# Kernel optimization log

Measured on AMD Instinct MI355X. Metric: run time of the kernel, lower is better.

## Reference

```python
import jax, jax.numpy as jnp
import numpy as np

EMBED = 1024
HEADS = 16
HEAD_DIM = EMBED // HEADS
B, S = 2, 2048


def setup_inputs() -> dict:
    key = jax.random.key(0)
    ks = jax.random.split(key, 9)
    std = 1.0 / np.sqrt(EMBED)
    def lin(k):
        kw, kb = jax.random.split(k)
        W = jax.random.uniform(kw, (EMBED, EMBED), jnp.float32, -std, std)
        b = jax.random.uniform(kb, (EMBED,), jnp.float32, -std, std)
        return W, b
    Wq, bq = lin(ks[0])
    Wk, bk = lin(ks[1])
    Wv, bv = lin(ks[2])
    Wo, bo = lin(ks[3])
    x = jax.random.normal(ks[4], (B, S, EMBED), jnp.float32)
    return {"x": x, "Wq": Wq, "bq": bq, "Wk": Wk, "bk": bk,
            "Wv": Wv, "bv": bv, "Wo": Wo, "bo": bo}


def reference(x, Wq, bq, Wk, bk, Wv, bv, Wo, bo):
    b, s, e = x.shape
    # projections (torch Linear: x @ W^T + b; here W stored as [in,out])
    Q = x @ Wq + bq
    K = x @ Wk + bk
    V = x @ Wv + bv
    # [b, h, s, d]
    Q = Q.reshape(b, s, HEADS, HEAD_DIM).transpose(0, 2, 1, 3)
    K = K.reshape(b, s, HEADS, HEAD_DIM).transpose(0, 2, 1, 3)
    V = V.reshape(b, s, HEADS, HEAD_DIM).transpose(0, 2, 1, 3)
    scores = jnp.einsum('bhqd,bhkd->bhqk', Q, K) / np.sqrt(HEAD_DIM)
    # causal mask: positions k > q masked to -inf
    causal = jnp.tril(jnp.ones((s, s), dtype=bool))
    scores = jnp.where(causal[None, None], scores, -jnp.inf)
    weights = jax.nn.softmax(scores, axis=-1)
    out = jnp.einsum('bhqk,bhkd->bhqd', weights, V)
    out = out.transpose(0, 2, 1, 3).reshape(b, s, e)
    return out @ Wo + bo
```

## Files before the change

### kernel.cpp

```cpp
#include <hip/hip_runtime.h>
#include <hip/hip_bf16.h>
#include <stdint.h>

#define EMBED 1024
#define HEADS 16
#define HDIM 64
#define BATCH 2
#define SEQ 2048
#define NROWS (BATCH*SEQ)

typedef __attribute__((ext_vector_type(8))) short short8;
typedef __attribute__((ext_vector_type(4))) float f32x4;

#define LOG2E 1.44269504088896f

__device__ __forceinline__ unsigned short f2bf(float f) {
    __hip_bfloat16 b = __float2bfloat16(f);
    return *reinterpret_cast<unsigned short*>(&b);
}

__device__ __forceinline__ unsigned cvt_pk_bf16(float lo, float hi) {
    unsigned r;
    asm("v_cvt_pk_bf16_f32 %0, %1, %2" : "=v"(r) : "v"(lo), "v"(hi));
    return r;
}

__device__ __forceinline__ short8 mk8(unsigned a, unsigned b, unsigned c, unsigned d) {
    union { unsigned u[4]; short8 s; } x;
    x.u[0] = a; x.u[1] = b; x.u[2] = c; x.u[3] = d;
    return x.s;
}

__device__ __forceinline__ void g2l16(const void* g, void* l) {
    __builtin_amdgcn_global_load_lds(
        (const __attribute__((address_space(1))) unsigned int*)g,
        (__attribute__((address_space(3))) unsigned int*)l, 16, 0, 0);
}

__global__ void cast_x_kernel(const float* __restrict__ x,
                              unsigned short* __restrict__ xb, int n4) {
    int i = blockIdx.x * blockDim.x + threadIdx.x;
    if (i < n4) {
        float4 v = reinterpret_cast<const float4*>(x)[i];
        ushort4 o;
        o.x = f2bf(v.x); o.y = f2bf(v.y); o.z = f2bf(v.z); o.w = f2bf(v.w);
        reinterpret_cast<ushort4*>(xb)[i] = o;
    }
}

__global__ void transW4_kernel(const float* __restrict__ W0,
                               const float* __restrict__ W1,
                               const float* __restrict__ W2,
                               const float* __restrict__ W3,
                               unsigned short* __restrict__ dst) {
    __shared__ float tile[32][33];
    const int z = blockIdx.z;
    const float* W = (z == 0) ? W0 : (z == 1) ? W1 : (z == 2) ? W2 : W3;
    unsigned short* Wt = dst + (size_t)z * EMBED * EMBED;
    int tx = threadIdx.x, ty = threadIdx.y;
#pragma unroll
    for (int r = 0; r < 4; r++) {
        int i = blockIdx.y * 32 + ty + r * 8;
        int o = blockIdx.x * 32 + tx;
        tile[ty + r * 8][tx] = W[(size_t)i * EMBED + o];
    }
    __syncthreads();
    int i2 = blockIdx.y * 32 + tx;
#pragma unroll
    for (int r = 0; r < 4; r++) {
        int o2 = blockIdx.x * 32 + ty + r * 8;
        Wt[(size_t)o2 * EMBED + i2] = f2bf(tile[tx][ty + r * 8]);
    }
}

template<int MODE, int BM>
__global__ __launch_bounds__(256)
void gemm_kernel(const unsigned short* __restrict__ A,
                 const unsigned short* __restrict__ B,
                 int K,
                 unsigned short* __restrict__ Qo,
                 unsigned short* __restrict__ Ko,
                 unsigned short* __restrict__ Vto,
                 const float* __restrict__ bq,
                 const float* __restrict__ bk,
                 const float* __restrict__ bvv,
                 float* __restrict__ Co,
                 const float* __restrict__ bo) {
    constexpr int AI = BM / 32;
    __shared__ __attribute__((aligned(16))) unsigned short As[BM * 64];
    __shared__ __attribute__((aligned(16))) unsigned short Bs[128 * 64];
    const int t = threadIdx.x;
    const int lane = t & 63;
    const int w = t >> 6;
    const int wr = w >> 1, wc = w & 1;
    const int l15 = lane & 15, l16 = lane >> 4;
    const int m0 = blockIdx.y * BM;
    const int n0 = blockIdx.x * 128;

    f32x4 acc[AI][4];
#pragma unroll
    for (int i = 0; i < AI; i++)
#pragma unroll
        for (int j = 0; j < 4; j++) acc[i][j] = (f32x4){0.f, 0.f, 0.f, 0.f};

    for (int k0 = 0; k0 < K; k0 += 64) {
        __syncthreads();
#pragma unroll
        for (int i = 0; i < BM / 32; i++) {
            int c = i * 256 + t;
            int row = c >> 3;
            int lc = (c & 7) ^ (row & 7);
            g2l16(A + (size_t)(m0 + row) * K + k0 + lc * 8,
                  As + (size_t)(i * 256 + (t & ~63)) * 8);
        }
#pragma unroll
        for (int i = 0; i < 4; i++) {
            int c = i * 256 + t;
            int row = c >> 3;
            int lc = (c & 7) ^ (row & 7);
            g2l16(B + (size_t)(n0 + row) * K + k0 + lc * 8,
                  Bs + (size_t)(i * 256 + (t & ~63)) * 8);
        }
        __syncthreads();
#pragma unroll
        for (int kk = 0; kk < 2; kk++) {
            short8 a[AI], b[4];
#pragma unroll
            for (int ai = 0; ai < AI; ai++) {
                int row = wr * (BM / 2) + ai * 16 + l15;
                int ch = kk * 4 + l16;
                a[ai] = *reinterpret_cast<const short8*>(
                    As + row * 64 + ((ch ^ (row & 7)) << 3));
            }
#pragma unroll
            for (int bj = 0; bj < 4; bj++) {
                int row = wc * 64 + bj * 16 + l15;
                int ch = kk * 4 + l16;
                b[bj] = *reinterpret_cast<const short8*>(
                    Bs + row * 64 + ((ch ^ (row & 7)) << 3));
            }
            __builtin_amdgcn_s_setprio(1);
#pragma unroll
            for (int ai = 0; ai < AI; ai++)
#pragma unroll
                for (int bj = 0; bj < 4; bj++)
                    acc[ai][bj] = __builtin_amdgcn_mfma_f32_16x16x32_bf16(
                        a[ai], b[bj], acc[ai][bj], 0, 0, 0);
            __builtin_amdgcn_s_setprio(0);
        }
    }

    if (MODE == 0) {
        const int which = n0 >> 10;
        const int coln = n0 & 1023;
        const float* bias = which == 0 ? bq : (which == 1 ? bk : bvv);
        const float scale = which == 0 ? 0.125f * LOG2E : 1.0f;
#pragma unroll
        for (int ai = 0; ai < AI; ai++) {
            int rowb = m0 + wr * (BM / 2) + ai * 16 + l16 * 4;
            int b_ = rowb >> 11;
            int s = rowb & 2047;
#pragma unroll
            for (int bj = 0; bj < 4; bj++) {
                int col = coln + wc * 64 + bj * 16 + l15;
                float bsv = bias[col];
                int h = col >> 6, d = col & 63;
                if (which < 2) {
                    unsigned short* dst = (which == 0) ? Qo : Ko;
                    size_t base = ((size_t)(b_ * HEADS + h)) * SEQ * HDIM;
#pragma unroll
                    for (int r = 0; r < 4; r++) {
                        float v = (acc[ai][bj][r] + bsv) * scale;
                        dst[base + (size_t)(s + r) * HDIM + d] = f2bf(v);
                    }
                } else {
                    ushort4 pk;
                    pk.x = f2bf(acc[ai][bj][0] + bsv);
                    pk.y = f2bf(acc[ai][bj][1] + bsv);
                    pk.z = f2bf(acc[ai][bj][2] + bsv);
                    pk.w = f2bf(acc[ai][bj][3] + bsv);
                    int cs = (s >> 2) & 15;
                    int ps = (cs & 8) | ((cs & 3) << 1) | ((cs >> 2) & 1);
                    size_t off = ((size_t)(b_ * HEADS + h) * HDIM + d) * SEQ +
                                 (size_t)((s & ~63) | (ps << 2));
                    *reinterpret_cast<ushort4*>(Vto + off) = pk;
                }
            }
        }
    } else {
#pragma unroll
        for (int ai = 0; ai < AI; ai++) {
            int rowb = m0 + wr * (BM / 2) + ai * 16 + l16 * 4;
#pragma unroll
            for (int bj = 0; bj < 4; bj++) {
                int col = n0 + wc * 64 + bj * 16 + l15;
                float bsv = bo[col];
#pragma unroll
                for (int r = 0; r < 4; r++)
                    Co[(size_t)(rowb + r) * EMBED + col] = acc[ai][bj][r] + bsv;
            }
        }
    }
}

__device__ __forceinline__ void stage_kv(const unsigned short* __restrict__ Kg,
                                         const unsigned short* __restrict__ Vg,
                                         int kv0, unsigned short* Ksb,
                                         unsigned short* Vsb, int tl) {
#pragma unroll
    for (int i = 0; i < 4; i++) {
        int c = i * 128 + tl;
        int row = c >> 3;
        int lc = (c & 7) ^ (row & 7);
        g2l16(Kg + (size_t)(kv0 + row) * HDIM + lc * 8,
              Ksb + (i * 128 + (tl & ~63)) * 8);
    }
#pragma unroll
    for (int i = 0; i < 4; i++) {
        int c = i * 128 + tl;
        int d = c >> 3;
        int lc = (c & 7) ^ (d & 7);
        g2l16(Vg + (size_t)d * SEQ + kv0 + lc * 8,
              Vsb + (i * 128 + (tl & ~63)) * 8);
    }
}

__global__ __launch_bounds__(256, 2)
void attn_kernel(const unsigned short* __restrict__ Q,
                 const unsigned short* __restrict__ Kk,
                 const unsigned short* __restrict__ Vt,
                 unsigned short* __restrict__ O) {
    __shared__ __attribute__((aligned(16))) unsigned short Ks[4][64 * 64];
    __shared__ __attribute__((aligned(16))) unsigned short Vs[4][64 * 64];

    const int t = threadIdx.x;
    const int lane = t & 63;
    const int w = t >> 6;
    const int wq = w >> 1;
    const int wk = w & 1;
    const int l15 = lane & 15, l16 = lane >> 4;

    const int id = blockIdx.x;
    const int xcd = id & 7;
    const int u = id >> 3;
    const int bh = xcd * 4 + (u & 3);
    const int su = u >> 2;
    const int qi = (su < 16) ? su : 47 - su;
    const int q0 = qi * 64;
    const size_t base = (size_t)bh * SEQ * HDIM;
    const unsigned short* Kg = Kk + base;
    const unsigned short* Vg = Vt + base;
    const int qrow0 = q0 + wq * 32;

    short8 qf[2][2];
    {
        const unsigned short* Qg = Q + base + (size_t)qrow0 * HDIM;
#pragma unroll
        for (int qb = 0; qb < 2; qb++)
#pragma unroll
            for (int kc = 0; kc < 2; kc++)
                qf[qb][kc] = *reinterpret_cast<const short8*>(
                    Qg + (qb * 16 + l15) * HDIM + (kc * 4 + l16) * 8);
    }

    f32x4 oacc[2][4];
#pragma unroll
    for (int qb = 0; qb < 2; qb++)
#pragma unroll
        for (int nd = 0; nd < 4; nd++) oacc[qb][nd] = (f32x4){0.f, 0.f, 0.f, 0.f};
    float m_run[2] = {-1e30f, -1e30f};
    float l_run[2] = {0.f, 0.f};

    const int nt = qi + 1;
    const int nsuper = (nt + 1) >> 1;

    auto stagepair = [&](int ta, int tb) {
        if (t < 128) {
            if (ta < nt) stage_kv(Kg, Vg, ta * 64, Ks[ta & 3], Vs[ta & 3], t);
        } else {
            if (tb < nt) stage_kv(Kg, Vg, tb * 64, Ks[tb & 3], Vs[tb & 3], t - 128);
        }
    };

    auto qkt = [&](f32x4 (&sc)[2][4], const unsigned short* Kb) {
#pragma unroll
        for (int qb = 0; qb < 2; qb++)
#pragma unroll
            for (int kb = 0; kb < 4; kb++) sc[qb][kb] = (f32x4){0.f, 0.f, 0.f, 0.f};
#pragma unroll
        for (int kc = 0; kc < 2; kc++) {
            short8 ka[4];
#pragma unroll
            for (int kb = 0; kb < 4; kb++) {
                int row = kb * 16 + l15;
                ka[kb] = *reinterpret_cast<const short8*>(
                    Kb + row * 64 + (((kc * 4 + l16) ^ (row & 7)) << 3));
            }
            __builtin_amdgcn_s_setprio(1);
#pragma unroll
            for (int qb = 0; qb < 2; qb++)
#pragma unroll
                for (int kb = 0; kb < 4; kb++)
                    sc[qb][kb] = __builtin_amdgcn_mfma_f32_16x16x32_bf16(
                        ka[kb], qf[qb][kc], sc[qb][kb], 0, 0, 0);
            __builtin_amdgcn_s_setprio(0);
        }
    };

    auto softmax_pv = [&](f32x4 (&sc)[2][4], const unsigned short* Vb, bool diag) {
        if (diag) {
#pragma unroll
            for (int qb = 0; qb < 2; qb++) {
                const int qloc = wq * 32 + qb * 16 + l15;
#pragma unroll
                for (int kb = 0; kb < 4; kb++)
#pragma unroll
                    for (int r = 0; r < 4; r++) {
                        int kloc = kb * 16 + l16 * 4 + r;
                        sc[qb][kb][r] = (kloc > qloc) ? -1e30f : sc[qb][kb][r];
                    }
            }
        }
        float vmax[2];
        bool need = false;
#pragma unroll
        for (int qb = 0; qb < 2; qb++) {
            float mx = -1e30f;
#pragma unroll
            for (int kb = 0; kb < 4; kb++)
                mx = fmaxf(mx, fmaxf(fmaxf(sc[qb][kb][0], sc[qb][kb][1]),
                                     fmaxf(sc[qb][kb][2], sc[qb][kb][3])));
            mx = fmaxf(mx, __shfl_xor(mx, 16));
            mx = fmaxf(mx, __shfl_xor(mx, 32));
            vmax[qb] = mx;
            need = need || (mx > m_run[qb] + 8.0f);
        }
        if (__any(need)) {
#pragma unroll
            for (int qb = 0; qb < 2; qb++) {
                float mn = fmaxf(m_run[qb], vmax[qb]);
                float sf = __builtin_amdgcn_exp2f(m_run[qb] - mn);
                m_run[qb] = mn;
                l_run[qb] *= sf;
#pragma unroll
                for (int r = 0; r < 4; r++) {
                    float sfr = __shfl(sf, l16 * 4 + r);
#pragma unroll
                    for (int nd = 0; nd < 4; nd++) oacc[qb][nd][r] *= sfr;
                }
            }
        }
        short8 pa[2][2];
#pragma unroll
        for (int qb = 0; qb < 2; qb++) {
            float p[4][4];
            float ps = 0.f;
#pragma unroll
            for (int kb = 0; kb < 4; kb++)
#pragma unroll
                for (int r = 0; r < 4; r++) {
                    p[kb][r] = __builtin_amdgcn_exp2f(sc[qb][kb][r] - m_run[qb]);
                    ps += p[kb][r];
                }
            pa[qb][0] = mk8(cvt_pk_bf16(p[0][0], p[0][1]),
                            cvt_pk_bf16(p[0][2], p[0][3]),
                            cvt_pk_bf16(p[1][0], p[1][1]),
                            cvt_pk_bf16(p[1][2], p[1][3]));
            pa[qb][1] = mk8(cvt_pk_bf16(p[2][0], p[2][1]),
                            cvt_pk_bf16(p[2][2], p[2][3]),
                            cvt_pk_bf16(p[3][0], p[3][1]),
                            cvt_pk_bf16(p[3][2], p[3][3]));
            ps += __shfl_xor(ps, 16);
            ps += __shfl_xor(ps, 32);
            l_run[qb] += ps;
        }
#pragma unroll
        for (int m = 0; m < 2; m++) {
            short8 vb[4];
#pragma unroll
            for (int nd = 0; nd < 4; nd++) {
                int row = nd * 16 + l15;
                vb[nd] = *reinterpret_cast<const short8*>(
                    Vb + row * 64 + (((m * 4 + l16) ^ (row & 7)) << 3));
            }
            __builtin_amdgcn_s_setprio(1);
#pragma unroll
            for (int qb = 0; qb < 2; qb++)
#pragma unroll
                for (int nd = 0; nd < 4; nd++)
                    oacc[qb][nd] = __builtin_amdgcn_mfma_f32_16x16x32_bf16(
                        pa[qb][m], vb[nd], oacc[qb][nd], 0, 0, 0);
            __builtin_amdgcn_s_setprio(0);
        }
    };

    f32x4 sc[2][4];

    stagepair(0, 1);
    asm volatile("s_waitcnt vmcnt(0)" ::: "memory");
    __builtin_amdgcn_s_barrier();
    asm volatile("" ::: "memory");
    stagepair(2, 3);
    int myt = wk;
    if (myt < nt) qkt(sc, Ks[myt & 3]);

    for (int j = 1; j < nsuper; j++) {
        if (myt < nt) softmax_pv(sc, Vs[myt & 3], false);
        asm volatile("s_waitcnt vmcnt(0)" ::: "memory");
        __builtin_amdgcn_s_barrier();
        asm volatile("" ::: "memory");
        stagepair(2 * j + 2, 2 * j + 3);
        int tc = 2 * j + wk;
        if (tc < nt) qkt(sc, Ks[tc & 3]);
        myt = tc;
    }
    if (myt < nt) softmax_pv(sc, Vs[myt & 3], myt == nt - 1);

    __syncthreads();
    float* po = reinterpret_cast<float*>(&Ks[0][0]);
    float* pml = reinterpret_cast<float*>(&Vs[0][0]);
    if (wk == 1) {
#pragma unroll
        for (int qb = 0; qb < 2; qb++) {
#pragma unroll
            for (int nd = 0; nd < 4; nd++)
                reinterpret_cast<f32x4*>(po)[(((wq << 1) | qb) * 4 + nd) * 64 + lane] =
                    oacc[qb][nd];
            pml[((((wq << 1) | qb) * 64) + lane) * 2]     = m_run[qb];
            pml[((((wq << 1) | qb) * 64) + lane) * 2 + 1] = l_run[qb];
        }
    }
    __syncthreads();
    if (wk == 0) {
        const int b_ = bh >> 4, h = bh & 15;
#pragma unroll
        for (int qb = 0; qb < 2; qb++) {
            float m1 = pml[((((wq << 1) | qb) * 64) + lane) * 2];
            float l1 = pml[((((wq << 1) | qb) * 64) + lane) * 2 + 1];
            float ms = fmaxf(m_run[qb], m1);
            float a0 = __builtin_amdgcn_exp2f(m_run[qb] - ms);
            float a1 = __builtin_amdgcn_exp2f(m1 - ms);
            float lm = l_run[qb] * a0 + l1 * a1;
            f32x4 o1[4];
#pragma unroll
            for (int nd = 0; nd < 4; nd++)
                o1[nd] = reinterpret_cast<f32x4*>(po)[(((wq << 1) | qb) * 4 + nd) * 64 + lane];
            float li = 1.0f / lm;
#pragma unroll
            for (int r = 0; r < 4; r++) {
                float a0r = __shfl(a0, l16 * 4 + r);
                float a1r = __shfl(a1, l16 * 4 + r);
                float lir = __shfl(li, l16 * 4 + r);
                int row = b_ * SEQ + qrow0 + qb * 16 + l16 * 4 + r;
#pragma unroll
                for (int nd = 0; nd < 4; nd++) {
                    float v = oacc[qb][nd][r] * a0r + o1[nd][r] * a1r;
                    O[(size_t)row * EMBED + h * 64 + nd * 16 + l15] = f2bf(v * lir);
                }
            }
        }
    }
}

extern "C" void kernel_launch(void* const* d_in, const int* in_sizes, int n_in,
                              void* d_out, int out_size, void* d_ws, size_t ws_size,
                              hipStream_t stream) {
    (void)in_sizes; (void)n_in; (void)out_size; (void)ws_size;
    const float* x  = (const float*)d_in[0];
    const float* Wq = (const float*)d_in[1];
    const float* bq = (const float*)d_in[2];
    const float* Wk = (const float*)d_in[3];
    const float* bk = (const float*)d_in[4];
    const float* Wv = (const float*)d_in[5];
    const float* bv = (const float*)d_in[6];
    const float* Wo = (const float*)d_in[7];
    const float* bo = (const float*)d_in[8];
    float* out = (float*)d_out;

    unsigned short* xb   = (unsigned short*)d_ws;
    unsigned short* Wqkv = xb + (size_t)NROWS * EMBED;
    unsigned short* Wot  = Wqkv + (size_t)3 * EMBED * EMBED;
    unsigned short* Qb   = Wot + (size_t)EMBED * EMBED;
    unsigned short* Kb   = Qb + (size_t)NROWS * EMBED;
    unsigned short* Vtb  = Kb + (size_t)NROWS * EMBED;
    unsigned short* attn = Vtb + (size_t)NROWS * EMBED;

    cast_x_kernel<<<(NROWS * EMBED / 4 + 255) / 256, 256, 0, stream>>>(
        x, xb, NROWS * EMBED / 4);
    transW4_kernel<<<dim3(32, 32, 4), dim3(32, 8), 0, stream>>>(
        Wq, Wk, Wv, Wo, Wqkv);

    gemm_kernel<0, 128><<<dim3(24, 32), 256, 0, stream>>>(
        xb, Wqkv, EMBED, Qb, Kb, Vtb, bq, bk, bv, nullptr, nullptr);

    attn_kernel<<<1024, 256, 0, stream>>>(Qb, Kb, Vtb, attn);

    gemm_kernel<1, 64><<<dim3(8, 64), 256, 0, stream>>>(
        attn, Wot, EMBED, nullptr, nullptr, nullptr, nullptr, nullptr, nullptr,
        out, bo);
}
```

Before: 98.74 us.

## Enlarge attention query tile to 128 rows with 512-thread blocks

The attention kernel now processes 128 query rows per block with 8 waves instead of 64 rows with 4 waves, so each staged K/V tile is reused by twice as many queries. This halves the total K/V global traffic and the number of blocks. Causal masking now uses global indices and skips per-wave tiles that lie entirely above the diagonal. The launch bounds ask for 4 blocks of 512 threads per CU, which may force a low VGPR budget and cause spills. The larger per-block causal work also gives the grid coarser load balance.

```diff
diff --git a/kernel.cpp b/kernel.cpp
--- a/kernel.cpp
+++ b/kernel.cpp
@@ -208,24 +208,24 @@
                                          int kv0, unsigned short* Ksb,
                                          unsigned short* Vsb, int tl) {
 #pragma unroll
-    for (int i = 0; i < 4; i++) {
-        int c = i * 128 + tl;
+    for (int i = 0; i < 2; i++) {
+        int c = i * 256 + tl;
         int row = c >> 3;
         int lc = (c & 7) ^ (row & 7);
         g2l16(Kg + (size_t)(kv0 + row) * HDIM + lc * 8,
-              Ksb + (i * 128 + (tl & ~63)) * 8);
-    }
-#pragma unroll
-    for (int i = 0; i < 4; i++) {
-        int c = i * 128 + tl;
+              Ksb + (i * 256 + (tl & ~63)) * 8);
+    }
+#pragma unroll
+    for (int i = 0; i < 2; i++) {
+        int c = i * 256 + tl;
         int d = c >> 3;
         int lc = (c & 7) ^ (d & 7);
         g2l16(Vg + (size_t)d * SEQ + kv0 + lc * 8,
-              Vsb + (i * 128 + (tl & ~63)) * 8);
-    }
-}
-
-__global__ __launch_bounds__(256, 2)
+              Vsb + (i * 256 + (tl & ~63)) * 8);
+    }
+}
+
+__global__ __launch_bounds__(512, 4)
 void attn_kernel(const unsigned short* __restrict__ Q,
                  const unsigned short* __restrict__ Kk,
                  const unsigned short* __restrict__ Vt,
@@ -245,8 +245,8 @@
     const int u = id >> 3;
     const int bh = xcd * 4 + (u & 3);
     const int su = u >> 2;
-    const int qi = (su < 16) ? su : 47 - su;
-    const int q0 = qi * 64;
+    const int qi = (su < 8) ? su : 23 - su;
+    const int q0 = qi * 128;
     const size_t base = (size_t)bh * SEQ * HDIM;
     const unsigned short* Kg = Kk + base;
     const unsigned short* Vg = Vt + base;
@@ -271,14 +271,14 @@
     float m_run[2] = {-1e30f, -1e30f};
     float l_run[2] = {0.f, 0.f};
 
-    const int nt = qi + 1;
-    const int nsuper = (nt + 1) >> 1;
+    const int nt = 2 * qi + 2;
+    const int nsuper = nt >> 1;
 
     auto stagepair = [&](int ta, int tb) {
-        if (t < 128) {
+        if (t < 256) {
             if (ta < nt) stage_kv(Kg, Vg, ta * 64, Ks[ta & 3], Vs[ta & 3], t);
         } else {
-            if (tb < nt) stage_kv(Kg, Vg, tb * 64, Ks[tb & 3], Vs[tb & 3], t - 128);
+            if (tb < nt) stage_kv(Kg, Vg, tb * 64, Ks[tb & 3], Vs[tb & 3], t - 256);
         }
     };
 
@@ -307,17 +307,17 @@
         }
     };
 
-    auto softmax_pv = [&](f32x4 (&sc)[2][4], const unsigned short* Vb, bool diag) {
-        if (diag) {
+    auto softmax_pv = [&](f32x4 (&sc)[2][4], const unsigned short* Vb, int kv0) {
+        if (kv0 + 63 > qrow0) {
 #pragma unroll
             for (int qb = 0; qb < 2; qb++) {
-                const int qloc = wq * 32 + qb * 16 + l15;
+                const int qg = qrow0 + qb * 16 + l15;
 #pragma unroll
                 for (int kb = 0; kb < 4; kb++)
 #pragma unroll
                     for (int r = 0; r < 4; r++) {
-                        int kloc = kb * 16 + l16 * 4 + r;
-                        sc[qb][kb][r] = (kloc > qloc) ? -1e30f : sc[qb][kb][r];
+                        int kg = kv0 + kb * 16 + l16 * 4 + r;
+                        sc[qb][kb][r] = (kg > qg) ? -1e30f : sc[qb][kb][r];
                     }
             }
         }
@@ -402,19 +402,21 @@
     asm volatile("" ::: "memory");
     stagepair(2, 3);
     int myt = wk;
-    if (myt < nt) qkt(sc, Ks[myt & 3]);
+    bool act = (myt < nt) && (myt * 64 <= qrow0 + 31);
+    if (act) qkt(sc, Ks[myt & 3]);
 
     for (int j = 1; j < nsuper; j++) {
-        if (myt < nt) softmax_pv(sc, Vs[myt & 3], false);
+        if (act) softmax_pv(sc, Vs[myt & 3], myt * 64);
         asm volatile("s_waitcnt vmcnt(0)" ::: "memory");
         __builtin_amdgcn_s_barrier();
         asm volatile("" ::: "memory");
         stagepair(2 * j + 2, 2 * j + 3);
         int tc = 2 * j + wk;
-        if (tc < nt) qkt(sc, Ks[tc & 3]);
+        act = (tc < nt) && (tc * 64 <= qrow0 + 31);
+        if (act) qkt(sc, Ks[tc & 3]);
         myt = tc;
     }
-    if (myt < nt) softmax_pv(sc, Vs[myt & 3], myt == nt - 1);
+    if (act) softmax_pv(sc, Vs[myt & 3], myt * 64);
 
     __syncthreads();
     float* po = reinterpret_cast<float*>(&Ks[0][0]);
@@ -422,12 +424,13 @@
     if (wk == 1) {
 #pragma unroll
         for (int qb = 0; qb < 2; qb++) {
+            int g = (wq << 1) | qb;
 #pragma unroll
             for (int nd = 0; nd < 4; nd++)
-                reinterpret_cast<f32x4*>(po)[(((wq << 1) | qb) * 4 + nd) * 64 + lane] =
+                reinterpret_cast<f32x4*>(po)[(g * 4 + nd) * 64 + lane] =
                     oacc[qb][nd];
-            pml[((((wq << 1) | qb) * 64) + lane) * 2]     = m_run[qb];
-            pml[((((wq << 1) | qb) * 64) + lane) * 2 + 1] = l_run[qb];
+            pml[(g * 64 + lane) * 2]     = m_run[qb];
+            pml[(g * 64 + lane) * 2 + 1] = l_run[qb];
         }
     }
     __syncthreads();
@@ -435,8 +438,9 @@
         const int b_ = bh >> 4, h = bh & 15;
 #pragma unroll
         for (int qb = 0; qb < 2; qb++) {
-            float m1 = pml[((((wq << 1) | qb) * 64) + lane) * 2];
-            float l1 = pml[((((wq << 1) | qb) * 64) + lane) * 2 + 1];
+            int g = (wq << 1) | qb;
+            float m1 = pml[(g * 64 + lane) * 2];
+            float l1 = pml[(g * 64 + lane) * 2 + 1];
             float ms = fmaxf(m_run[qb], m1);
             float a0 = __builtin_amdgcn_exp2f(m_run[qb] - ms);
             float a1 = __builtin_amdgcn_exp2f(m1 - ms);
@@ -444,7 +448,7 @@
             f32x4 o1[4];
 #pragma unroll
             for (int nd = 0; nd < 4; nd++)
-                o1[nd] = reinterpret_cast<f32x4*>(po)[(((wq << 1) | qb) * 4 + nd) * 64 + lane];
+                o1[nd] = reinterpret_cast<f32x4*>(po)[(g * 4 + nd) * 64 + lane];
             float li = 1.0f / lm;
 #pragma unroll
             for (int r = 0; r < 4; r++) {
@@ -493,7 +497,7 @@
     gemm_kernel<0, 128><<<dim3(24, 32), 256, 0, stream>>>(
         xb, Wqkv, EMBED, Qb, Kb, Vtb, bq, bk, bv, nullptr, nullptr);
 
-    attn_kernel<<<1024, 256, 0, stream>>>(Qb, Kb, Vtb, attn);
+    attn_kernel<<<512, 512, 0, stream>>>(Qb, Kb, Vtb, attn);
 
     gemm_kernel<1, 64><<<dim3(8, 64), 256, 0, stream>>>(
         attn, Wot, EMBED, nullptr, nullptr, nullptr, nullptr, nullptr, nullptr,
```

Result: slower. 155.3 us (+57.3%).
